# Kernel tuning notes

Measured on AMD Instinct MI355X. Metric: run time of the kernel, lower is better.

## Reference

```python
import jax, jax.numpy as jnp
import numpy as np

N_CHANNELS = 29
HIDDEN = [5, 4, 4]
IN_FEAT = 7
OUT_FEAT = 3
EPS = 1e-07


def _glorot(key, fan_in, fan_out, shape):
    lim = np.sqrt(6.0 / (fan_in + fan_out))
    return jax.random.uniform(key, shape, jnp.float32, -lim, lim)


def _make_params(key):
    # Batched per-channel weights: stack n_channels tiny MLPs along leading dim.
    sizes = [IN_FEAT] + HIDDEN + [OUT_FEAT]
    Ws, bs = [], []
    for i in range(len(sizes) - 1):
        key, k = jax.random.split(key)
        Ws.append(_glorot(k, sizes[i], sizes[i + 1], (N_CHANNELS, sizes[i], sizes[i + 1])))
        bs.append(jnp.zeros((N_CHANNELS, sizes[i + 1]), jnp.float32))
    return Ws, bs


def setup_inputs() -> dict:
    key = jax.random.key(0)
    ks = jax.random.split(key, 16)
    N = 262144
    inp = {
        "tau": jax.random.uniform(ks[0], (N, N_CHANNELS, 1), jnp.float32),
        "mu": jax.random.uniform(ks[1], (N, 1), jnp.float32, 0.05, 1.0),
        "mu_bar": jax.random.uniform(ks[2], (N, 1), jnp.float32, 0.05, 1.0),
        "lw": jax.random.uniform(ks[3], (N, 1), jnp.float32),
        "h2o": jax.random.uniform(ks[4], (N, 1), jnp.float32),
        "o3": jax.random.uniform(ks[5], (N, 1), jnp.float32),
        "co2": jax.random.uniform(ks[6], (N, 1), jnp.float32),
        "u": jax.random.uniform(ks[7], (N, 1), jnp.float32),
        "n2o": jax.random.uniform(ks[8], (N, 1), jnp.float32),
        "ch4": jax.random.uniform(ks[9], (N, 1), jnp.float32),
    }
    Wd, bd = _make_params(ks[10])
    Wf, bf = _make_params(ks[11])
    for i in range(4):
        inp[f"Wd{i}"] = Wd[i]
        inp[f"bd{i}"] = bd[i]
        inp[f"Wf{i}"] = Wf[i]
        inp[f"bf{i}"] = bf[i]
    return inp


def _mlp(x, Ws, bs):
    # x: [N, F]; Ws[i]: [C, fin, fout]; output [N, C, 3]
    h = jnp.einsum('nf,cfh->nch', x, Ws[0]) + bs[0]
    h = jax.nn.relu(h)
    for i in (1, 2):
        h = jnp.einsum('nch,chk->nck', h, Ws[i]) + bs[i]
        h = jax.nn.relu(h)
    h = jnp.einsum('nch,chk->nck', h, Ws[3]) + bs[3]
    return jax.nn.softmax(h, axis=-1)


def reference(tau, mu, mu_bar, lw, h2o, o3, co2, u, n2o, ch4,
              Wd0, bd0, Wd1, bd1, Wd2, bd2, Wd3, bd3,
              Wf0, bf0, Wf1, bf1, Wf2, bf2, Wf3, bf3):
    constituents = jnp.concatenate([lw, h2o, o3, co2, u, n2o, ch4], axis=1)  # [N,7]
    c_direct = constituents / (mu + EPS)
    c_diffuse = constituents / (mu_bar + EPS)
    mu3 = mu[:, :, None]          # [N,1,1]
    mu_bar3 = mu_bar[:, :, None]
    tau_total = jnp.sum(tau, axis=-1, keepdims=True)  # [N,C,1]
    t_direct = jnp.exp(-tau_total / (mu3 + EPS))       # [N,C,1]
    t_diffuse = jnp.exp(-tau_total / (mu_bar3 + EPS))
    e_direct = _mlp(c_direct, [Wd0, Wd1, Wd2, Wd3], [bd0, bd1, bd2, bd3])    # [N,C,3]
    e_diffuse = _mlp(c_diffuse, [Wf0, Wf1, Wf2, Wf3], [bf0, bf1, bf2, bf3])  # [N,C,3]
    return jnp.concatenate([t_direct, t_diffuse, e_direct, e_diffuse], axis=2)  # [N,C,8]
```

## Files before the change

kernel.cpp:

```cpp
#include <hip/hip_runtime.h>

#define EPS 1e-7f
#define NCH 29
#define SPB 64
#define ROWF4 59


__device__ __forceinline__ void barrier_lds_only() {
    asm volatile("s_waitcnt lgkmcnt(0)\n\ts_barrier" ::: "memory");
}

__device__ __forceinline__ void mlp7(const float x[7],
    const float* __restrict__ W0, const float* __restrict__ b0,
    const float* __restrict__ W1, const float* __restrict__ b1,
    const float* __restrict__ W2, const float* __restrict__ b2,
    const float* __restrict__ W3, const float* __restrict__ b3,
    float e[3])
{
    float h0[5];
#pragma unroll
    for (int h = 0; h < 5; ++h) {
        float a = b0[h];
#pragma unroll
        for (int f = 0; f < 7; ++f) a = fmaf(x[f], W0[f * 5 + h], a);
        h0[h] = fmaxf(a, 0.0f);
    }
    float h1[4];
#pragma unroll
    for (int k = 0; k < 4; ++k) {
        float a = b1[k];
#pragma unroll
        for (int h = 0; h < 5; ++h) a = fmaf(h0[h], W1[h * 4 + k], a);
        h1[k] = fmaxf(a, 0.0f);
    }
    float h2[4];
#pragma unroll
    for (int k = 0; k < 4; ++k) {
        float a = b2[k];
#pragma unroll
        for (int h = 0; h < 4; ++h) a = fmaf(h1[h], W2[h * 4 + k], a);
        h2[k] = fmaxf(a, 0.0f);
    }
    float l[3];
#pragma unroll
    for (int k = 0; k < 3; ++k) {
        float a = b3[k];
#pragma unroll
        for (int h = 0; h < 4; ++h) a = fmaf(h2[h], W3[h * 3 + k], a);
        l[k] = a;
    }
    float m = fmaxf(l[0], fmaxf(l[1], l[2]));
    float e0 = __expf(l[0] - m);
    float e1 = __expf(l[1] - m);
    float e2 = __expf(l[2] - m);
    float rs = __builtin_amdgcn_rcpf(e0 + e1 + e2);
    e[0] = e0 * rs; e[1] = e1 * rs; e[2] = e2 * rs;
}

__global__ __launch_bounds__(512, 4) void lps_kernel(
    const float* __restrict__ tau, const float* __restrict__ mu, const float* __restrict__ mu_bar,
    const float* __restrict__ lw, const float* __restrict__ h2o, const float* __restrict__ o3,
    const float* __restrict__ co2, const float* __restrict__ uu, const float* __restrict__ n2o,
    const float* __restrict__ ch4,
    const float* __restrict__ Wd0, const float* __restrict__ bd0,
    const float* __restrict__ Wf0, const float* __restrict__ bf0,
    const float* __restrict__ Wd1, const float* __restrict__ bd1,
    const float* __restrict__ Wf1, const float* __restrict__ bf1,
    const float* __restrict__ Wd2, const float* __restrict__ bd2,
    const float* __restrict__ Wf2, const float* __restrict__ bf2,
    const float* __restrict__ Wd3, const float* __restrict__ bd3,
    const float* __restrict__ Wf3, const float* __restrict__ bf3,
    float* __restrict__ out, int N)
{
    __shared__ __align__(16) float4 obuf[SPB * ROWF4];

    const int tid  = threadIdx.x;
    const int lane = tid & 63;
    const int wid  = __builtin_amdgcn_readfirstlane(tid >> 6);

    const long long base = (long long)blockIdx.x * SPB;
    const int s0 = (int)base + lane;
    const int i0 = (s0 < N) ? s0 : (N - 1);

    const float rmu  = __builtin_amdgcn_rcpf(mu[i0] + EPS);
    const float rmub = __builtin_amdgcn_rcpf(mu_bar[i0] + EPS);
    const float nrmu  = -rmu;
    const float nrmub = -rmub;

    float cons[7];
    cons[0] = lw[i0]; cons[1] = h2o[i0]; cons[2] = o3[i0]; cons[3] = co2[i0];
    cons[4] = uu[i0]; cons[5] = n2o[i0]; cons[6] = ch4[i0];

    float xd[7], xf[7];
#pragma unroll
    for (int f = 0; f < 7; ++f) { xd[f] = cons[f] * rmu; xf[f] = cons[f] * rmub; }

    const float* taun = tau + (size_t)i0 * NCH;

#pragma unroll
    for (int it = 0; it < 4; ++it) {
        const int c = wid + it * 8;
        if (c < NCH) {
            const float tv = taun[c];
            const float t_dir = __expf(tv * nrmu);
            const float t_dif = __expf(tv * nrmub);

            float ed[3], ef[3];
            mlp7(xd, Wd0 + c * 35, bd0 + c * 5, Wd1 + c * 20, bd1 + c * 4,
                     Wd2 + c * 16, bd2 + c * 4, Wd3 + c * 12, bd3 + c * 3, ed);
            mlp7(xf, Wf0 + c * 35, bf0 + c * 5, Wf1 + c * 20, bf1 + c * 4,
                     Wf2 + c * 16, bf2 + c * 4, Wf3 + c * 12, bf3 + c * 3, ef);

            obuf[lane * ROWF4 + c * 2]     = make_float4(t_dir, t_dif, ed[0], ed[1]);
            obuf[lane * ROWF4 + c * 2 + 1] = make_float4(ed[2], ef[0], ef[1], ef[2]);
        }
    }

    barrier_lds_only();

    float4* out4 = (float4*)out;
    int nsamp = N - (int)base;
    if (nsamp > SPB) nsamp = SPB;
    if (nsamp > 0) {
        const int tot = nsamp * 58;
        const long long ob = base * 58;
        for (int i = tid; i < tot; i += 512) {
            const int s = i / 58, r = i - s * 58;
            out4[ob + i] = obuf[s * ROWF4 + r];
        }
    }
}

extern "C" void kernel_launch(void* const* d_in, const int* in_sizes, int n_in,
                              void* d_out, int out_size, void* d_ws, size_t ws_size,
                              hipStream_t stream) {
    const float* tau    = (const float*)d_in[0];
    const float* mu     = (const float*)d_in[1];
    const float* mu_bar = (const float*)d_in[2];
    const float* lw     = (const float*)d_in[3];
    const float* h2o    = (const float*)d_in[4];
    const float* o3     = (const float*)d_in[5];
    const float* co2    = (const float*)d_in[6];
    const float* uu     = (const float*)d_in[7];
    const float* n2o    = (const float*)d_in[8];
    const float* ch4    = (const float*)d_in[9];

    const float* Wd0 = (const float*)d_in[10];
    const float* bd0 = (const float*)d_in[11];
    const float* Wf0 = (const float*)d_in[12];
    const float* bf0 = (const float*)d_in[13];
    const float* Wd1 = (const float*)d_in[14];
    const float* bd1 = (const float*)d_in[15];
    const float* Wf1 = (const float*)d_in[16];
    const float* bf1 = (const float*)d_in[17];
    const float* Wd2 = (const float*)d_in[18];
    const float* bd2 = (const float*)d_in[19];
    const float* Wf2 = (const float*)d_in[20];
    const float* bf2 = (const float*)d_in[21];
    const float* Wd3 = (const float*)d_in[22];
    const float* bd3 = (const float*)d_in[23];
    const float* Wf3 = (const float*)d_in[24];
    const float* bf3 = (const float*)d_in[25];

    float* out = (float*)d_out;
    int N = in_sizes[1];

    int blocks = (N + SPB - 1) / SPB;
    lps_kernel<<<blocks, 512, 0, stream>>>(
        tau, mu, mu_bar, lw, h2o, o3, co2, uu, n2o, ch4,
        Wd0, bd0, Wf0, bf0, Wd1, bd1, Wf1, bf1,
        Wd2, bd2, Wf2, bf2, Wd3, bd3, Wf3, bf3,
        out, N);
}
```

Before: 92.86 us.

## Split LDS output staging into two halves to cut shared memory and raise occupancy

The output staging buffer is halved: channels 0-15 are computed, staged and written out first, then the buffer is reused for channels 16-28. This shrinks LDS per block from about 60KB to about 34KB, so more blocks can be resident, and the launch bound minimum-blocks hint goes from 4 to 6. In exchange there is an extra barrier and an extra store phase, and the stores for each sample are now split into two partially coalesced segments instead of one contiguous stream.

```diff
diff --git a/kernel.cpp b/kernel.cpp
--- a/kernel.cpp
+++ b/kernel.cpp
@@ -3,7 +3,7 @@
 #define EPS 1e-7f
 #define NCH 29
 #define SPB 64
-#define ROWF4 59
+#define ROWA 33
 
 
 __device__ __forceinline__ void barrier_lds_only() {
@@ -57,7 +57,7 @@
     e[0] = e0 * rs; e[1] = e1 * rs; e[2] = e2 * rs;
 }
 
-__global__ __launch_bounds__(512, 4) void lps_kernel(
+__global__ __launch_bounds__(512, 6) void lps_kernel(
     const float* __restrict__ tau, const float* __restrict__ mu, const float* __restrict__ mu_bar,
     const float* __restrict__ lw, const float* __restrict__ h2o, const float* __restrict__ o3,
     const float* __restrict__ co2, const float* __restrict__ uu, const float* __restrict__ n2o,
@@ -72,7 +72,7 @@
     const float* __restrict__ Wf3, const float* __restrict__ bf3,
     float* __restrict__ out, int N)
 {
-    __shared__ __align__(16) float4 obuf[SPB * ROWF4];
+    __shared__ __align__(16) float4 obuf[SPB * ROWA];
 
     const int tid  = threadIdx.x;
     const int lane = tid & 63;
@@ -97,8 +97,39 @@
 
     const float* taun = tau + (size_t)i0 * NCH;
 
-#pragma unroll
-    for (int it = 0; it < 4; ++it) {
+    int nsamp = N - (int)base;
+    if (nsamp > SPB) nsamp = SPB;
+    float4* out4 = (float4*)out;
+
+#pragma unroll
+    for (int it = 0; it < 2; ++it) {
+        const int c = wid + it * 8;
+        const float tv = taun[c];
+        const float t_dir = __expf(tv * nrmu);
+        const float t_dif = __expf(tv * nrmub);
+
+        float ed[3], ef[3];
+        mlp7(xd, Wd0 + c * 35, bd0 + c * 5, Wd1 + c * 20, bd1 + c * 4,
+                 Wd2 + c * 16, bd2 + c * 4, Wd3 + c * 12, bd3 + c * 3, ed);
+        mlp7(xf, Wf0 + c * 35, bf0 + c * 5, Wf1 + c * 20, bf1 + c * 4,
+                 Wf2 + c * 16, bf2 + c * 4, Wf3 + c * 12, bf3 + c * 3, ef);
+
+        obuf[lane * ROWA + c * 2]     = make_float4(t_dir, t_dif, ed[0], ed[1]);
+        obuf[lane * ROWA + c * 2 + 1] = make_float4(ed[2], ef[0], ef[1], ef[2]);
+    }
+
+    barrier_lds_only();
+    if (nsamp > 0) {
+        const int tot = nsamp * 32;
+        for (int i = tid; i < tot; i += 512) {
+            const int s = i >> 5, r = i & 31;
+            out4[(base + s) * 58 + r] = obuf[s * ROWA + r];
+        }
+    }
+    barrier_lds_only();
+
+#pragma unroll
+    for (int it = 2; it < 4; ++it) {
         const int c = wid + it * 8;
         if (c < NCH) {
             const float tv = taun[c];
@@ -111,22 +142,18 @@
             mlp7(xf, Wf0 + c * 35, bf0 + c * 5, Wf1 + c * 20, bf1 + c * 4,
                      Wf2 + c * 16, bf2 + c * 4, Wf3 + c * 12, bf3 + c * 3, ef);
 
-            obuf[lane * ROWF4 + c * 2]     = make_float4(t_dir, t_dif, ed[0], ed[1]);
-            obuf[lane * ROWF4 + c * 2 + 1] = make_float4(ed[2], ef[0], ef[1], ef[2]);
+            const int slot = (c - 16) * 2;
+            obuf[lane * ROWA + slot]     = make_float4(t_dir, t_dif, ed[0], ed[1]);
+            obuf[lane * ROWA + slot + 1] = make_float4(ed[2], ef[0], ef[1], ef[2]);
         }
     }
 
     barrier_lds_only();
-
-    float4* out4 = (float4*)out;
-    int nsamp = N - (int)base;
-    if (nsamp > SPB) nsamp = SPB;
     if (nsamp > 0) {
-        const int tot = nsamp * 58;
-        const long long ob = base * 58;
+        const int tot = nsamp * 26;
         for (int i = tid; i < tot; i += 512) {
-            const int s = i / 58, r = i - s * 58;
-            out4[ob + i] = obuf[s * ROWF4 + r];
+            const int s = i / 26, r = i - s * 26;
+            out4[(base + s) * 58 + 32 + r] = obuf[s * ROWA + r];
         }
     }
 }
```

Result: faster. 89.67 us (-3.4%).

## Process two samples per lane and split direct/diffuse MLPs across waves

Applied to the files above, without the earlier changes.

Doubles the samples per block to 128 and launches 1024 threads. Each wave now owns one (channel, direct-or-diffuse) pair and runs that one MLP for two samples per lane, so each wave-uniform weight load is shared by two FMA chains. The goal is to amortise scalar weight-load overhead and add instruction-level parallelism. In exchange the LDS staging buffer grows to about 118 KB per block, which leaves room for only one block per CU, and the output rows are now written with partial scalar LDS stores.

```diff
diff --git a/kernel.cpp b/kernel.cpp
--- a/kernel.cpp
+++ b/kernel.cpp
@@ -2,7 +2,7 @@
 
 #define EPS 1e-7f
 #define NCH 29
-#define SPB 64
+#define SPB 128
 #define ROWF4 59
 
 
@@ -10,54 +10,7 @@
     asm volatile("s_waitcnt lgkmcnt(0)\n\ts_barrier" ::: "memory");
 }
 
-__device__ __forceinline__ void mlp7(const float x[7],
-    const float* __restrict__ W0, const float* __restrict__ b0,
-    const float* __restrict__ W1, const float* __restrict__ b1,
-    const float* __restrict__ W2, const float* __restrict__ b2,
-    const float* __restrict__ W3, const float* __restrict__ b3,
-    float e[3])
-{
-    float h0[5];
-#pragma unroll
-    for (int h = 0; h < 5; ++h) {
-        float a = b0[h];
-#pragma unroll
-        for (int f = 0; f < 7; ++f) a = fmaf(x[f], W0[f * 5 + h], a);
-        h0[h] = fmaxf(a, 0.0f);
-    }
-    float h1[4];
-#pragma unroll
-    for (int k = 0; k < 4; ++k) {
-        float a = b1[k];
-#pragma unroll
-        for (int h = 0; h < 5; ++h) a = fmaf(h0[h], W1[h * 4 + k], a);
-        h1[k] = fmaxf(a, 0.0f);
-    }
-    float h2[4];
-#pragma unroll
-    for (int k = 0; k < 4; ++k) {
-        float a = b2[k];
-#pragma unroll
-        for (int h = 0; h < 4; ++h) a = fmaf(h1[h], W2[h * 4 + k], a);
-        h2[k] = fmaxf(a, 0.0f);
-    }
-    float l[3];
-#pragma unroll
-    for (int k = 0; k < 3; ++k) {
-        float a = b3[k];
-#pragma unroll
-        for (int h = 0; h < 4; ++h) a = fmaf(h2[h], W3[h * 3 + k], a);
-        l[k] = a;
-    }
-    float m = fmaxf(l[0], fmaxf(l[1], l[2]));
-    float e0 = __expf(l[0] - m);
-    float e1 = __expf(l[1] - m);
-    float e2 = __expf(l[2] - m);
-    float rs = __builtin_amdgcn_rcpf(e0 + e1 + e2);
-    e[0] = e0 * rs; e[1] = e1 * rs; e[2] = e2 * rs;
-}
-
-__global__ __launch_bounds__(512, 4) void lps_kernel(
+__global__ __launch_bounds__(1024, 4) void lps_kernel(
     const float* __restrict__ tau, const float* __restrict__ mu, const float* __restrict__ mu_bar,
     const float* __restrict__ lw, const float* __restrict__ h2o, const float* __restrict__ o3,
     const float* __restrict__ co2, const float* __restrict__ uu, const float* __restrict__ n2o,
@@ -80,39 +33,119 @@
 
     const long long base = (long long)blockIdx.x * SPB;
     const int s0 = (int)base + lane;
+    const int s1 = s0 + 64;
     const int i0 = (s0 < N) ? s0 : (N - 1);
-
-    const float rmu  = __builtin_amdgcn_rcpf(mu[i0] + EPS);
-    const float rmub = __builtin_amdgcn_rcpf(mu_bar[i0] + EPS);
-    const float nrmu  = -rmu;
-    const float nrmub = -rmub;
-
-    float cons[7];
-    cons[0] = lw[i0]; cons[1] = h2o[i0]; cons[2] = o3[i0]; cons[3] = co2[i0];
-    cons[4] = uu[i0]; cons[5] = n2o[i0]; cons[6] = ch4[i0];
-
-    float xd[7], xf[7];
-#pragma unroll
-    for (int f = 0; f < 7; ++f) { xd[f] = cons[f] * rmu; xf[f] = cons[f] * rmub; }
-
-    const float* taun = tau + (size_t)i0 * NCH;
-
-#pragma unroll
-    for (int it = 0; it < 4; ++it) {
-        const int c = wid + it * 8;
-        if (c < NCH) {
-            const float tv = taun[c];
-            const float t_dir = __expf(tv * nrmu);
-            const float t_dif = __expf(tv * nrmub);
-
-            float ed[3], ef[3];
-            mlp7(xd, Wd0 + c * 35, bd0 + c * 5, Wd1 + c * 20, bd1 + c * 4,
-                     Wd2 + c * 16, bd2 + c * 4, Wd3 + c * 12, bd3 + c * 3, ed);
-            mlp7(xf, Wf0 + c * 35, bf0 + c * 5, Wf1 + c * 20, bf1 + c * 4,
-                     Wf2 + c * 16, bf2 + c * 4, Wf3 + c * 12, bf3 + c * 3, ef);
-
-            obuf[lane * ROWF4 + c * 2]     = make_float4(t_dir, t_dif, ed[0], ed[1]);
-            obuf[lane * ROWF4 + c * 2 + 1] = make_float4(ed[2], ef[0], ef[1], ef[2]);
+    const int i1 = (s1 < N) ? s1 : (N - 1);
+    const int l0 = lane, l1 = lane + 64;
+
+    const float rmu0  = __builtin_amdgcn_rcpf(mu[i0] + EPS);
+    const float rmu1  = __builtin_amdgcn_rcpf(mu[i1] + EPS);
+    const float rmub0 = __builtin_amdgcn_rcpf(mu_bar[i0] + EPS);
+    const float rmub1 = __builtin_amdgcn_rcpf(mu_bar[i1] + EPS);
+
+    float cons0[7], cons1[7];
+    cons0[0] = lw[i0];  cons1[0] = lw[i1];
+    cons0[1] = h2o[i0]; cons1[1] = h2o[i1];
+    cons0[2] = o3[i0];  cons1[2] = o3[i1];
+    cons0[3] = co2[i0]; cons1[3] = co2[i1];
+    cons0[4] = uu[i0];  cons1[4] = uu[i1];
+    cons0[5] = n2o[i0]; cons1[5] = n2o[i1];
+    cons0[6] = ch4[i0]; cons1[6] = ch4[i1];
+
+#pragma unroll
+    for (int p = 0; p < 4; ++p) {
+        const int r = p * 16 + wid;
+        if (r < 2 * NCH) {
+            const int c  = r >> 1;
+            const int ty = r & 1;
+
+            const float* __restrict__ W0 = (ty ? Wf0 : Wd0) + c * 35;
+            const float* __restrict__ B0 = (ty ? bf0 : bd0) + c * 5;
+            const float* __restrict__ W1 = (ty ? Wf1 : Wd1) + c * 20;
+            const float* __restrict__ B1 = (ty ? bf1 : bd1) + c * 4;
+            const float* __restrict__ W2 = (ty ? Wf2 : Wd2) + c * 16;
+            const float* __restrict__ B2 = (ty ? bf2 : bd2) + c * 4;
+            const float* __restrict__ W3 = (ty ? Wf3 : Wd3) + c * 12;
+            const float* __restrict__ B3 = (ty ? bf3 : bd3) + c * 3;
+
+            const float rs0 = ty ? rmub0 : rmu0;
+            const float rs1 = ty ? rmub1 : rmu1;
+
+            float x0[7], x1[7];
+#pragma unroll
+            for (int f = 0; f < 7; ++f) { x0[f] = cons0[f] * rs0; x1[f] = cons1[f] * rs1; }
+
+            float h0a[5], h0b[5];
+#pragma unroll
+            for (int h = 0; h < 5; ++h) {
+                float a = B0[h], b = B0[h];
+#pragma unroll
+                for (int f = 0; f < 7; ++f) {
+                    const float w = W0[f * 5 + h];
+                    a = fmaf(x0[f], w, a);
+                    b = fmaf(x1[f], w, b);
+                }
+                h0a[h] = fmaxf(a, 0.0f); h0b[h] = fmaxf(b, 0.0f);
+            }
+            float h1a[4], h1b[4];
+#pragma unroll
+            for (int k = 0; k < 4; ++k) {
+                float a = B1[k], b = B1[k];
+#pragma unroll
+                for (int f = 0; f < 5; ++f) {
+                    const float w = W1[f * 4 + k];
+                    a = fmaf(h0a[f], w, a);
+                    b = fmaf(h0b[f], w, b);
+                }
+                h1a[k] = fmaxf(a, 0.0f); h1b[k] = fmaxf(b, 0.0f);
+            }
+            float h2a[4], h2b[4];
+#pragma unroll
+            for (int k = 0; k < 4; ++k) {
+                float a = B2[k], b = B2[k];
+#pragma unroll
+                for (int f = 0; f < 4; ++f) {
+                    const float w = W2[f * 4 + k];
+                    a = fmaf(h1a[f], w, a);
+                    b = fmaf(h1b[f], w, b);
+                }
+                h2a[k] = fmaxf(a, 0.0f); h2b[k] = fmaxf(b, 0.0f);
+            }
+            float la[3], lb[3];
+#pragma unroll
+            for (int k = 0; k < 3; ++k) {
+                float a = B3[k], b = B3[k];
+#pragma unroll
+                for (int f = 0; f < 4; ++f) {
+                    const float w = W3[f * 3 + k];
+                    a = fmaf(h2a[f], w, a);
+                    b = fmaf(h2b[f], w, b);
+                }
+                la[k] = a; lb[k] = b;
+            }
+            const float ma = fmaxf(la[0], fmaxf(la[1], la[2]));
+            const float mb = fmaxf(lb[0], fmaxf(lb[1], lb[2]));
+            const float ea0 = __expf(la[0] - ma), ea1 = __expf(la[1] - ma), ea2 = __expf(la[2] - ma);
+            const float eb0 = __expf(lb[0] - mb), eb1 = __expf(lb[1] - mb), eb2 = __expf(lb[2] - mb);
+            const float ra = __builtin_amdgcn_rcpf(ea0 + ea1 + ea2);
+            const float rb = __builtin_amdgcn_rcpf(eb0 + eb1 + eb2);
+
+            if (ty == 0) {
+                const float tv0 = tau[(size_t)i0 * NCH + c];
+                const float tv1 = tau[(size_t)i1 * NCH + c];
+                const float td0 = __expf(-tv0 * rmu0), tf0 = __expf(-tv0 * rmub0);
+                const float td1 = __expf(-tv1 * rmu1), tf1 = __expf(-tv1 * rmub1);
+
+                obuf[l0 * ROWF4 + 2 * c] = make_float4(td0, tf0, ea0 * ra, ea1 * ra);
+                ((float*)&obuf[l0 * ROWF4 + 2 * c + 1])[0] = ea2 * ra;
+                obuf[l1 * ROWF4 + 2 * c] = make_float4(td1, tf1, eb0 * rb, eb1 * rb);
+                ((float*)&obuf[l1 * ROWF4 + 2 * c + 1])[0] = eb2 * rb;
+            } else {
+                float* q0 = (float*)&obuf[l0 * ROWF4 + 2 * c + 1];
+                q0[1] = ea0 * ra; q0[2] = ea1 * ra; q0[3] = ea2 * ra;
+                float* q1 = (float*)&obuf[l1 * ROWF4 + 2 * c + 1];
+                q1[1] = eb0 * rb; q1[2] = eb1 * rb; q1[3] = eb2 * rb;
+            }
         }
     }
 
@@ -124,9 +157,9 @@
     if (nsamp > 0) {
         const int tot = nsamp * 58;
         const long long ob = base * 58;
-        for (int i = tid; i < tot; i += 512) {
-            const int s = i / 58, r = i - s * 58;
-            out4[ob + i] = obuf[s * ROWF4 + r];
+        for (int i = tid; i < tot; i += 1024) {
+            const int s = i / 58, rr = i - s * 58;
+            out4[ob + i] = obuf[s * ROWF4 + rr];
         }
     }
 }
@@ -166,7 +199,7 @@
     int N = in_sizes[1];
 
     int blocks = (N + SPB - 1) / SPB;
-    lps_kernel<<<blocks, 512, 0, stream>>>(
+    lps_kernel<<<blocks, 1024, 0, stream>>>(
         tau, mu, mu_bar, lw, h2o, o3, co2, uu, n2o, ch4,
         Wd0, bd0, Wf0, bf0, Wd1, bd1, Wf1, bf1,
         Wd2, bd2, Wf2, bf2, Wd3, bd3, Wf3, bf3,
```

New measurement: 104.2 us. 1.12x slower.
